# Kernel tuning notes

Hardware: AMD Instinct MI355X
Metric: run time of the kernel (lower is better)

The kernel has to match this reference:

```python
import jax, jax.numpy as jnp
import numpy as np

N = 100000      # nodes
E = 1600000     # edges (avg degree 16)
D_IN = 128
D_H = 128
D_OUT = 2


def setup_inputs() -> dict:
    key = jax.random.key(0)
    ks = jax.random.split(key, 13)
    s = 0.05
    x = jax.random.normal(ks[0], (N, D_IN), jnp.float32)
    edge_src = jax.random.randint(ks[1], (E,), 0, N, jnp.int32)
    edge_dst = jax.random.randint(ks[2], (E,), 0, N, jnp.int32)
    # SAGEConv params per layer: lin_l (aggregated path, with bias), lin_r (root path)
    w_l0 = jax.random.normal(ks[3], (D_H, D_IN), jnp.float32) * s
    b0 = jnp.zeros((D_H,), jnp.float32)
    w_r0 = jax.random.normal(ks[4], (D_H, D_IN), jnp.float32) * s
    w_l1 = jax.random.normal(ks[5], (D_H, D_H), jnp.float32) * s
    b1 = jnp.zeros((D_H,), jnp.float32)
    w_r1 = jax.random.normal(ks[6], (D_H, D_H), jnp.float32) * s
    w_l2 = jax.random.normal(ks[7], (D_OUT, D_H), jnp.float32) * s
    b2 = jnp.zeros((D_OUT,), jnp.float32)
    w_r2 = jax.random.normal(ks[8], (D_OUT, D_H), jnp.float32) * s
    return {"x": x, "w_l0": w_l0, "b0": b0, "w_r0": w_r0,
            "w_l1": w_l1, "b1": b1, "w_r1": w_r1,
            "w_l2": w_l2, "b2": b2, "w_r2": w_r2,
            "edge_src": edge_src, "edge_dst": edge_dst}


def _sage_conv(h, src, dst, inv_deg, w_l, b, w_r):
    # mean aggregation of neighbor features: gather -> segment_sum -> scale
    agg = jax.ops.segment_sum(h[src], dst, num_segments=N) * inv_deg  # [N, d_in]
    return agg @ w_l.T + b + h @ w_r.T


def reference(x, w_l0, b0, w_r0, w_l1, b1, w_r1, w_l2, b2, w_r2, edge_src, edge_dst):
    # in-degree for mean aggregation (0-degree nodes -> mean of 0)
    deg = jax.ops.segment_sum(jnp.ones((E,), jnp.float32), edge_dst, num_segments=N)
    inv_deg = (1.0 / jnp.maximum(deg, 1.0))[:, None]  # [N, 1]
    h = jax.nn.relu(_sage_conv(x, edge_src, edge_dst, inv_deg, w_l0, b0, w_r0))
    # dropout is identity at inference (training=False)
    h = jax.nn.relu(_sage_conv(h, edge_src, edge_dst, inv_deg, w_l1, b1, w_r1))
    out = _sage_conv(h, edge_src, edge_dst, inv_deg, w_l2, b2, w_r2)
    return jax.nn.log_softmax(out, axis=1)
```

## Files before the change

### kernel.cpp

```cpp
#include <hip/hip_runtime.h>
#include <stdint.h>
#include <stddef.h>

#define DH 128
#define CHUNK 4096
#define NBKMAX 128

typedef short v8s __attribute__((ext_vector_type(8)));
typedef float v4f __attribute__((ext_vector_type(4)));

static __device__ __forceinline__ float bf2f(uint16_t h) {
    union { uint32_t i; float f; } u; u.i = ((uint32_t)h) << 16; return u.f;
}
static __device__ __forceinline__ uint16_t f2bf(float f) {
    union { float f; uint32_t i; } u; u.f = f;
    uint32_t r = u.i + 0x7fffu + ((u.i >> 16) & 1u);
    return (uint16_t)(r >> 16);
}
static __device__ __forceinline__ float loadf(const void* p, size_t i, bool f32) {
    return f32 ? ((const float*)p)[i] : bf2f(((const uint16_t*)p)[i]);
}

__global__ void init_k(const uint32_t* w, int* flag) {
    int t = threadIdx.x;
    int hits = 0;
    for (int k = 0; k < 4; ++k) {
        uint32_t u = w[t * 4 + k];
        int e = (u >> 7) & 0xFF;
        hits += (e >= 100 && e <= 130) ? 1 : 0;
    }
    for (int off = 32; off; off >>= 1) hits += __shfl_down(hits, off);
    if (t == 0) *flag = (hits >= 128) ? 0 : 1;
}

__global__ void cvtall_k(const void* x, const void* wl0, const void* wr0,
                         const void* wl1, const void* wr1, const void* b0,
                         const void* b1, const int* dt, uint16_t* xb,
                         uint16_t* wcvt, int nx) {
    int i = blockIdx.x * 256 + threadIdx.x;
    bool f32 = (*dt != 0);
    if (i < nx) {
        if (f32) xb[i] = f2bf(((const float*)x)[i]);
        return;
    }
    int j = i - nx;
    const void* src; int off;
    if      (j < 16384) { src = wl0; off = j; }
    else if (j < 32768) { src = wr0; off = j - 16384; }
    else if (j < 49152) { src = wl1; off = j - 32768; }
    else if (j < 65536) { src = wr1; off = j - 49152; }
    else if (j < 65664) { src = b0;  off = j - 65536; }
    else if (j < 65792) { src = b1;  off = j - 65664; }
    else return;
    wcvt[j] = f32 ? f2bf(((const float*)src)[off]) : ((const uint16_t*)src)[off];
}

__global__ void histA_k(const int* __restrict__ dst, int* gh,
                        int E, int n, int GH, int nbk) {
    __shared__ int h[NBKMAX];
    int t = threadIdx.x;
    int base = blockIdx.x * CHUNK;
    for (int i = t; i < NBKMAX; i += 256) h[i] = 0;
    __syncthreads();
    for (int it = 0; it < CHUNK / 256; ++it) {
        int e = base + it * 256 + t;
        if (e < E) {
            int d = dst[e];
            if ((unsigned)d < (unsigned)n) atomicAdd(&h[d >> 10], 1);
        }
    }
    __syncthreads();
    for (int b = t; b < nbk; b += 256) gh[b * GH + blockIdx.x] = h[b];
}

__global__ void scan1_k(const int* cnt, int* bsum, int n) {
    __shared__ int wt[4];
    int t = threadIdx.x, lane = t & 63, wv = t >> 6;
    int i = blockIdx.x * 256 + t;
    int v = (i < n) ? cnt[i] : 0;
    for (int off = 32; off; off >>= 1) v += __shfl_down(v, off);
    if (lane == 0) wt[wv] = v;
    __syncthreads();
    if (t == 0) bsum[blockIdx.x] = wt[0] + wt[1] + wt[2] + wt[3];
}

__global__ void scan2_k(const int* bsum, int* boff, int* row_n, int nb) {
    __shared__ int wt[4];
    __shared__ int carry_s;
    int t = threadIdx.x, lane = t & 63, wv = t >> 6;
    if (t == 0) carry_s = 0;
    __syncthreads();
    for (int base = 0; base < nb; base += 256) {
        int i = base + t;
        int c = (i < nb) ? bsum[i] : 0;
        int v = c;
        for (int off = 1; off < 64; off <<= 1) {
            int u = __shfl_up(v, off);
            if (lane >= off) v += u;
        }
        if (lane == 63) wt[wv] = v;
        __syncthreads();
        int woff = 0;
        for (int w = 0; w < wv; ++w) woff += wt[w];
        int total = wt[0] + wt[1] + wt[2] + wt[3];
        int carry = carry_s;
        if (i < nb) boff[i] = carry + woff + (v - c);
        __syncthreads();
        if (t == 0) carry_s = carry + total;
        __syncthreads();
    }
    if (t == 0) *row_n = carry_s;
}

__global__ void scanG3_k(const int* in, const int* boff, int* out, int n) {
    __shared__ int wt[4];
    int t = threadIdx.x, lane = t & 63, wv = t >> 6;
    int i = blockIdx.x * 256 + t;
    int c = (i < n) ? in[i] : 0;
    int v = c;
    for (int off = 1; off < 64; off <<= 1) {
        int u = __shfl_up(v, off);
        if (lane >= off) v += u;
    }
    if (lane == 63) wt[wv] = v;
    __syncthreads();
    int woff = 0;
    for (int w = 0; w < wv; ++w) woff += wt[w];
    if (i < n) out[i] = boff[blockIdx.x] + woff + (v - c);
}

__global__ void scatB_k(const int* __restrict__ src, const int* __restrict__ dst,
                        const int* __restrict__ ghs, uint32_t* gbuf,
                        int E, int n, int GH, int nbk) {
    __shared__ int cur[NBKMAX];
    int t = threadIdx.x;
    int base = blockIdx.x * CHUNK;
    for (int b = t; b < nbk; b += 256) cur[b] = ghs[b * GH + blockIdx.x];
    __syncthreads();
    for (int it = 0; it < CHUNK / 256; ++it) {
        int e = base + it * 256 + t;
        if (e < E) {
            int d = dst[e];
            if ((unsigned)d < (unsigned)n) {
                int s = src[e];
                int slot = atomicAdd(&cur[d >> 10], 1);
                uint32_t rec = ((uint32_t)(d & 1023) << 17) | (uint32_t)s;
                __builtin_nontemporal_store(rec, &gbuf[slot]);
            }
        }
    }
}

__global__ void regroupC_k(const uint32_t* __restrict__ gbuf, const int* ghs,
                           const int* __restrict__ totalp, int GH,
                           int* row_start, float* inv_deg, int* csr_src,
                           int n, int nbk) {
    __shared__ int lcnt[1024];
    __shared__ int rs[1024];
    __shared__ int wsum[4];
    int b = blockIdx.x, t = threadIdx.x, lane = t & 63, wv = t >> 6;
    int node0 = b << 10;
    int nn = n - node0; if (nn > 1024) nn = 1024;
    int start = ghs[b * GH];
    int end = (b + 1 < nbk) ? ghs[(b + 1) * GH] : *totalp;
    for (int i = t; i < 1024; i += 256) lcnt[i] = 0;
    __syncthreads();
    for (int i = start + t; i < end; i += 256)
        atomicAdd(&lcnt[gbuf[i] >> 17], 1);
    __syncthreads();
    int c0 = lcnt[t * 4], c1 = lcnt[t * 4 + 1], c2 = lcnt[t * 4 + 2], c3 = lcnt[t * 4 + 3];
    int s = c0 + c1 + c2 + c3;
    int v = s;
    for (int off = 1; off < 64; off <<= 1) {
        int u = __shfl_up(v, off);
        if (lane >= off) v += u;
    }
    if (lane == 63) wsum[wv] = v;
    __syncthreads();
    int woff = 0;
    for (int w = 0; w < wv; ++w) woff += wsum[w];
    int ex = woff + (v - s);
    rs[t * 4]     = ex;
    rs[t * 4 + 1] = ex + c0;
    rs[t * 4 + 2] = ex + c0 + c1;
    rs[t * 4 + 3] = ex + c0 + c1 + c2;
    __syncthreads();
    for (int i = t; i < nn; i += 256) {
        row_start[node0 + i] = start + rs[i];
        inv_deg[node0 + i] = 1.0f / fmaxf((float)lcnt[i], 1.0f);
    }
    __syncthreads();
    for (int i = t; i < 1024; i += 256) lcnt[i] = 0;
    __syncthreads();
    for (int i = start + t; i < end; i += 256) {
        uint32_t rec = gbuf[i];
        int local = rec >> 17;
        int sv = rec & 0x1FFFF;
        int rank = atomicAdd(&lcnt[local], 1);
        csr_src[start + rs[local] + rank] = sv;
    }
}

__global__ void agg_k(const uint16_t* feat, const uint16_t* feat_alt, const int* xdt,
                      const int* csr_src, const int* row_start, const float* inv_deg,
                      uint16_t* A, int n) {
    int wave = threadIdx.x >> 6, lane = threadIdx.x & 63;
    int node = blockIdx.x * 4 + wave;
    if (node >= n) return;
    const uint16_t* f = feat;
    if (xdt != nullptr && *xdt == 0) f = feat_alt;
    int seg = lane & 7, sub = lane >> 3;
    int e0 = row_start[node], e1 = row_start[node + 1];
    const uint4* fp = (const uint4*)f;
    float acc[16];
#pragma unroll
    for (int i = 0; i < 16; ++i) acc[i] = 0.f;
    for (int e = e0 + sub; e < e1; e += 8) {
        int s = csr_src[e];
        if ((unsigned)s >= (unsigned)n) continue;
        const uint4* row = fp + (size_t)s * 16 + seg * 2;
        uint4 u0 = row[0];
        uint4 u1 = row[1];
        acc[0]  += bf2f((uint16_t)u0.x); acc[1]  += bf2f((uint16_t)(u0.x >> 16));
        acc[2]  += bf2f((uint16_t)u0.y); acc[3]  += bf2f((uint16_t)(u0.y >> 16));
        acc[4]  += bf2f((uint16_t)u0.z); acc[5]  += bf2f((uint16_t)(u0.z >> 16));
        acc[6]  += bf2f((uint16_t)u0.w); acc[7]  += bf2f((uint16_t)(u0.w >> 16));
        acc[8]  += bf2f((uint16_t)u1.x); acc[9]  += bf2f((uint16_t)(u1.x >> 16));
        acc[10] += bf2f((uint16_t)u1.y); acc[11] += bf2f((uint16_t)(u1.y >> 16));
        acc[12] += bf2f((uint16_t)u1.z); acc[13] += bf2f((uint16_t)(u1.z >> 16));
        acc[14] += bf2f((uint16_t)u1.w); acc[15] += bf2f((uint16_t)(u1.w >> 16));
    }
#pragma unroll
    for (int i = 0; i < 16; ++i) {
        acc[i] += __shfl_down(acc[i], 32);
        acc[i] += __shfl_down(acc[i], 16);
        acc[i] += __shfl_down(acc[i], 8);
    }
    if (sub == 0) {
        float sc = inv_deg[node];
        uint4 o0, o1;
        o0.x = (uint32_t)f2bf(acc[0]*sc)  | ((uint32_t)f2bf(acc[1]*sc)  << 16);
        o0.y = (uint32_t)f2bf(acc[2]*sc)  | ((uint32_t)f2bf(acc[3]*sc)  << 16);
        o0.z = (uint32_t)f2bf(acc[4]*sc)  | ((uint32_t)f2bf(acc[5]*sc)  << 16);
        o0.w = (uint32_t)f2bf(acc[6]*sc)  | ((uint32_t)f2bf(acc[7]*sc)  << 16);
        o1.x = (uint32_t)f2bf(acc[8]*sc)  | ((uint32_t)f2bf(acc[9]*sc)  << 16);
        o1.y = (uint32_t)f2bf(acc[10]*sc) | ((uint32_t)f2bf(acc[11]*sc) << 16);
        o1.z = (uint32_t)f2bf(acc[12]*sc) | ((uint32_t)f2bf(acc[13]*sc) << 16);
        o1.w = (uint32_t)f2bf(acc[14]*sc) | ((uint32_t)f2bf(acc[15]*sc) << 16);
        uint4* dst = (uint4*)A + (size_t)node * 16 + seg * 2;
        dst[0] = o0;
        dst[1] = o1;
    }
}

__global__ void dense2_k(const uint16_t* __restrict__ X,
                         const uint16_t* __restrict__ Xalt, const int* xdt,
                         const uint16_t* __restrict__ A,
                         const uint16_t* __restrict__ Wr,
                         const uint16_t* __restrict__ Wl,
                         const uint16_t* __restrict__ bias,
                         uint16_t* __restrict__ H, int n) {
    const int lane = threadIdx.x & 63;
    const int wv = threadIdx.x >> 6;
    const int m0 = blockIdx.x * 128 + wv * 32;
    if (m0 >= n) return;
    const uint16_t* Xs = X;
    if (xdt != nullptr && *xdt == 0) Xs = Xalt;
    const int row16 = lane & 15, quad = lane >> 4;
    int mr0 = m0 + row16;      int ml0 = (mr0 < n) ? mr0 : (n - 1);
    int mr1 = m0 + 16 + row16; int ml1 = (mr1 < n) ? mr1 : (n - 1);
    v8s ax0[4], aa0[4], ax1[4], aa1[4];
    const uint16_t* xr0 = Xs + (size_t)ml0 * DH + quad * 8;
    const uint16_t* ar0 = A  + (size_t)ml0 * DH + quad * 8;
    const uint16_t* xr1 = Xs + (size_t)ml1 * DH + quad * 8;
    const uint16_t* ar1 = A  + (size_t)ml1 * DH + quad * 8;
#pragma unroll
    for (int kt = 0; kt < 4; ++kt) {
        ax0[kt] = *(const v8s*)(xr0 + kt * 32);
        aa0[kt] = *(const v8s*)(ar0 + kt * 32);
        ax1[kt] = *(const v8s*)(xr1 + kt * 32);
        aa1[kt] = *(const v8s*)(ar1 + kt * 32);
    }
#pragma unroll
    for (int nt = 0; nt < 8; ++nt) {
        v4f acc0 = {0.f, 0.f, 0.f, 0.f};
        v4f acc1 = {0.f, 0.f, 0.f, 0.f};
        const uint16_t* wrr = Wr + (size_t)(nt * 16 + row16) * DH + quad * 8;
        const uint16_t* wlr = Wl + (size_t)(nt * 16 + row16) * DH + quad * 8;
#pragma unroll
        for (int kt = 0; kt < 4; ++kt) {
            v8s br = *(const v8s*)(wrr + kt * 32);
            acc0 = __builtin_amdgcn_mfma_f32_16x16x32_bf16(ax0[kt], br, acc0, 0, 0, 0);
            acc1 = __builtin_amdgcn_mfma_f32_16x16x32_bf16(ax1[kt], br, acc1, 0, 0, 0);
            v8s bl = *(const v8s*)(wlr + kt * 32);
            acc0 = __builtin_amdgcn_mfma_f32_16x16x32_bf16(aa0[kt], bl, acc0, 0, 0, 0);
            acc1 = __builtin_amdgcn_mfma_f32_16x16x32_bf16(aa1[kt], bl, acc1, 0, 0, 0);
        }
        int o = nt * 16 + row16;
        float bo = bf2f(bias[o]);
#pragma unroll
        for (int r = 0; r < 4; ++r) {
            int m = m0 + quad * 4 + r;
            if (m < n)
                H[(size_t)m * DH + o] = f2bf(fmaxf(acc0[r] + bo, 0.0f));
            int m2 = m0 + 16 + quad * 4 + r;
            if (m2 < n)
                H[(size_t)m2 * DH + o] = f2bf(fmaxf(acc1[r] + bo, 0.0f));
        }
    }
}

__global__ void transform2_k(const uint16_t* H, const void* Wl2,
                             const void* Wr2, const int* wdt,
                             float* T, float* Q, int n) {
    int wave = threadIdx.x >> 6, lane = threadIdx.x & 63;
    int node = blockIdx.x * 4 + wave;
    if (node >= n) return;
    bool f32 = (*wdt != 0);
    const uint16_t* h = H + (size_t)node * DH;
    float h0 = bf2f(h[lane]), h1 = bf2f(h[lane + 64]);
    float p0 = h0 * loadf(Wl2, lane, f32)       + h1 * loadf(Wl2, 64 + lane, f32);
    float p1 = h0 * loadf(Wl2, 128 + lane, f32) + h1 * loadf(Wl2, 192 + lane, f32);
    float q0 = h0 * loadf(Wr2, lane, f32)       + h1 * loadf(Wr2, 64 + lane, f32);
    float q1 = h0 * loadf(Wr2, 128 + lane, f32) + h1 * loadf(Wr2, 192 + lane, f32);
    for (int off = 32; off; off >>= 1) {
        p0 += __shfl_down(p0, off);
        p1 += __shfl_down(p1, off);
        q0 += __shfl_down(q0, off);
        q1 += __shfl_down(q1, off);
    }
    if (lane == 0) {
        T[(size_t)node * 2]     = p0;
        T[(size_t)node * 2 + 1] = p1;
        Q[(size_t)node * 2]     = q0;
        Q[(size_t)node * 2 + 1] = q1;
    }
}

__global__ void final_k(const float* T, const float* Q, const int* row_start,
                        const int* csr_src, const float* inv_deg,
                        const void* b2, const int* wdt, float* out, int n) {
    int i = blockIdx.x * 256 + threadIdx.x;
    if (i >= n) return;
    bool f32 = (*wdt != 0);
    int e0 = row_start[i], e1 = row_start[i + 1];
    float s0 = 0.f, s1 = 0.f;
    for (int e = e0; e < e1; ++e) {
        int j = csr_src[e];
        if ((unsigned)j >= (unsigned)n) continue;
        s0 += T[(size_t)j * 2];
        s1 += T[(size_t)j * 2 + 1];
    }
    float sc = inv_deg[i];
    float l0 = s0 * sc + loadf(b2, 0, f32) + Q[(size_t)i * 2];
    float l1 = s1 * sc + loadf(b2, 1, f32) + Q[(size_t)i * 2 + 1];
    float m = fmaxf(l0, l1);
    float lse = m + logf(expf(l0 - m) + expf(l1 - m));
    out[(size_t)i * 2]     = l0 - lse;
    out[(size_t)i * 2 + 1] = l1 - lse;
}

extern "C" void kernel_launch(void* const* d_in, const int* in_sizes, int n_in,
                              void* d_out, int out_size, void* d_ws, size_t ws_size,
                              hipStream_t stream) {
    int ix, iwl0, ib0, iwr0, iwl1, ib1, iwr1, iwl2, ib2, iwr2, iesrc, iedst;
    if (in_sizes[0] < 100000) {
        ib0 = 0; ib1 = 1; ib2 = 2; iedst = 3; iesrc = 4;
        iwl0 = 5; iwl1 = 6; iwl2 = 7; iwr0 = 8; iwr1 = 9; iwr2 = 10; ix = 11;
    } else {
        ix = 0; iwl0 = 1; ib0 = 2; iwr0 = 3; iwl1 = 4; ib1 = 5;
        iwr1 = 6; iwl2 = 7; ib2 = 8; iwr2 = 9; iesrc = 10; iedst = 11;
    }
    const void* x   = d_in[ix];
    const void* wl0 = d_in[iwl0];
    const void* b0  = d_in[ib0];
    const void* wr0 = d_in[iwr0];
    const void* wl1 = d_in[iwl1];
    const void* b1  = d_in[ib1];
    const void* wr1 = d_in[iwr1];
    const void* wl2 = d_in[iwl2];
    const void* b2  = d_in[ib2];
    const void* wr2 = d_in[iwr2];
    const int* esrc = (const int*)d_in[iesrc];
    const int* edst = (const int*)d_in[iedst];
    const int N = out_size / 2;
    const int E = in_sizes[iesrc];
    (void)n_in; (void)ws_size;

    char* ws = (char*)d_ws;
    size_t off = 0;
    auto carve = [&](size_t bytes) -> char* {
        char* p = ws + off;
        off = (off + bytes + 255) & ~(size_t)255;
        return p;
    };
    int gN = (N + 255) / 256;
    int GH = (E + CHUNK - 1) / CHUNK;
    int nbk = (N + 1023) >> 10;
    int n_scan = nbk * GH;
    int gS = (n_scan + 255) / 256;
    int* dtf        = (int*)   carve(256);
    int* gh         = (int*)   carve((size_t)n_scan * 4);
    int* ghs        = (int*)   carve((size_t)n_scan * 4);
    int* bsum       = (int*)   carve((size_t)gS * 4);
    int* boff       = (int*)   carve((size_t)gS * 4);
    uint32_t* gbuf  = (uint32_t*)carve((size_t)E * 4);
    int* row_start  = (int*)   carve((size_t)(N + 1) * 4);
    float* inv_deg  = (float*) carve((size_t)N * 4);
    int* csr_src    = (int*)   carve((size_t)E * 4);
    uint16_t* A16   = (uint16_t*)carve((size_t)N * DH * 2);
    uint16_t* H16   = (uint16_t*)carve((size_t)N * DH * 2);
    uint16_t* xb    = (uint16_t*)carve((size_t)N * DH * 2);
    uint16_t* wcvt  = (uint16_t*)carve(65792 * 2);
    float* T        = (float*) carve((size_t)N * 2 * 4);
    float* Q        = (float*) carve((size_t)N * 2 * 4);
    uint16_t* wl0b = wcvt;
    uint16_t* wr0b = wcvt + 16384;
    uint16_t* wl1b = wcvt + 32768;
    uint16_t* wr1b = wcvt + 49152;
    uint16_t* b0b  = wcvt + 65536;
    uint16_t* b1b  = wcvt + 65664;

    int ga = (N + 3) / 4;
    int gd = (N + 127) / 128;
    int nx = N * DH;
    int gc = (nx + 65792 + 255) / 256;

    init_k<<<1, 64, 0, stream>>>((const uint32_t*)wl0, dtf);
    cvtall_k<<<gc, 256, 0, stream>>>(x, wl0, wr0, wl1, wr1, b0, b1, dtf, xb, wcvt, nx);

    histA_k<<<GH, 256, 0, stream>>>(edst, gh, E, N, GH, nbk);
    scan1_k<<<gS, 256, 0, stream>>>(gh, bsum, n_scan);
    scan2_k<<<1, 256, 0, stream>>>(bsum, boff, &row_start[N], gS);
    scanG3_k<<<gS, 256, 0, stream>>>(gh, boff, ghs, n_scan);
    scatB_k<<<GH, 256, 0, stream>>>(esrc, edst, ghs, gbuf, E, N, GH, nbk);
    regroupC_k<<<nbk, 256, 0, stream>>>(gbuf, ghs, &row_start[N], GH,
                                        row_start, inv_deg, csr_src, N, nbk);

    agg_k<<<ga, 256, 0, stream>>>(xb, (const uint16_t*)x, dtf,
                                  csr_src, row_start, inv_deg, A16, N);
    dense2_k<<<gd, 256, 0, stream>>>(xb, (const uint16_t*)x, dtf,
                                     A16, wr0b, wl0b, b0b, H16, N);

    agg_k<<<ga, 256, 0, stream>>>(H16, nullptr, nullptr,
                                  csr_src, row_start, inv_deg, A16, N);
    dense2_k<<<gd, 256, 0, stream>>>(H16, nullptr, nullptr,
                                     A16, wr1b, wl1b, b1b, H16, N);

    transform2_k<<<ga, 256, 0, stream>>>(H16, wl2, wr2, dtf, T, Q, N);
    final_k<<<gN, 256, 0, stream>>>(T, Q, row_start, csr_src, inv_deg,
                                    b2, dtf, (float*)d_out, N);
}
```

Baseline: 472.5 us.

## Fuse dtype probe, last-layer projection and conversions; shrink bucket size to 512

Result: slower. 517.6 us (+9.5%).

```diff
diff --git a/kernel.cpp b/kernel.cpp
--- a/kernel.cpp
+++ b/kernel.cpp
@@ -4,7 +4,8 @@
 
 #define DH 128
 #define CHUNK 4096
-#define NBKMAX 128
+#define PBK_SHIFT 9
+#define NBKMAX 224
 
 typedef short v8s __attribute__((ext_vector_type(8)));
 typedef float v4f __attribute__((ext_vector_type(4)));
@@ -21,44 +22,20 @@
     return f32 ? ((const float*)p)[i] : bf2f(((const uint16_t*)p)[i]);
 }
 
-__global__ void init_k(const uint32_t* w, int* flag) {
-    int t = threadIdx.x;
-    int hits = 0;
-    for (int k = 0; k < 4; ++k) {
-        uint32_t u = w[t * 4 + k];
-        int e = (u >> 7) & 0xFF;
-        hits += (e >= 100 && e <= 130) ? 1 : 0;
-    }
-    for (int off = 32; off; off >>= 1) hits += __shfl_down(hits, off);
-    if (t == 0) *flag = (hits >= 128) ? 0 : 1;
-}
-
-__global__ void cvtall_k(const void* x, const void* wl0, const void* wr0,
-                         const void* wl1, const void* wr1, const void* b0,
-                         const void* b1, const int* dt, uint16_t* xb,
-                         uint16_t* wcvt, int nx) {
-    int i = blockIdx.x * 256 + threadIdx.x;
-    bool f32 = (*dt != 0);
-    if (i < nx) {
-        if (f32) xb[i] = f2bf(((const float*)x)[i]);
-        return;
-    }
-    int j = i - nx;
-    const void* src; int off;
-    if      (j < 16384) { src = wl0; off = j; }
-    else if (j < 32768) { src = wr0; off = j - 16384; }
-    else if (j < 49152) { src = wl1; off = j - 32768; }
-    else if (j < 65536) { src = wr1; off = j - 49152; }
-    else if (j < 65664) { src = b0;  off = j - 65536; }
-    else if (j < 65792) { src = b1;  off = j - 65664; }
-    else return;
-    wcvt[j] = f32 ? f2bf(((const float*)src)[off]) : ((const uint16_t*)src)[off];
-}
-
-__global__ void histA_k(const int* __restrict__ dst, int* gh,
-                        int E, int n, int GH, int nbk) {
+__global__ void histA_k(const int* __restrict__ dst, const uint32_t* w, int* flag,
+                        int* gh, int E, int n, int GH, int nbk) {
     __shared__ int h[NBKMAX];
     int t = threadIdx.x;
+    if (blockIdx.x == 0 && t < 64) {
+        int hits = 0;
+        for (int k = 0; k < 4; ++k) {
+            uint32_t u = w[t * 4 + k];
+            int e = (u >> 7) & 0xFF;
+            hits += (e >= 100 && e <= 130) ? 1 : 0;
+        }
+        for (int off = 32; off; off >>= 1) hits += __shfl_down(hits, off);
+        if (t == 0) *flag = (hits >= 128) ? 0 : 1;
+    }
     int base = blockIdx.x * CHUNK;
     for (int i = t; i < NBKMAX; i += 256) h[i] = 0;
     __syncthreads();
@@ -66,11 +43,33 @@
         int e = base + it * 256 + t;
         if (e < E) {
             int d = dst[e];
-            if ((unsigned)d < (unsigned)n) atomicAdd(&h[d >> 10], 1);
+            if ((unsigned)d < (unsigned)n) atomicAdd(&h[d >> PBK_SHIFT], 1);
         }
     }
     __syncthreads();
     for (int b = t; b < nbk; b += 256) gh[b * GH + blockIdx.x] = h[b];
+}
+
+__global__ void cvtall_k(const void* x, const void* wl0, const void* wr0,
+                         const void* wl1, const void* wr1, const void* b0,
+                         const void* b1, const int* dt, uint16_t* xb,
+                         uint16_t* wcvt, int nx, int nthr) {
+    int i = blockIdx.x * 256 + threadIdx.x;
+    bool f32 = (*dt != 0);
+    if (i < 65792) {
+        const void* src; int off;
+        if      (i < 16384) { src = wl0; off = i; }
+        else if (i < 32768) { src = wr0; off = i - 16384; }
+        else if (i < 49152) { src = wl1; off = i - 32768; }
+        else if (i < 65536) { src = wr1; off = i - 49152; }
+        else if (i < 65664) { src = b0;  off = i - 65536; }
+        else                { src = b1;  off = i - 65664; }
+        wcvt[i] = f32 ? f2bf(((const float*)src)[off]) : ((const uint16_t*)src)[off];
+    }
+    if (f32) {
+        for (int k = i; k < nx; k += nthr)
+            xb[k] = f2bf(((const float*)x)[k]);
+    }
 }
 
 __global__ void scan1_k(const int* cnt, int* bsum, int n) {
@@ -143,8 +142,8 @@
             int d = dst[e];
             if ((unsigned)d < (unsigned)n) {
                 int s = src[e];
-                int slot = atomicAdd(&cur[d >> 10], 1);
-                uint32_t rec = ((uint32_t)(d & 1023) << 17) | (uint32_t)s;
+                int slot = atomicAdd(&cur[d >> PBK_SHIFT], 1);
+                uint32_t rec = ((uint32_t)(d & 511) << 17) | (uint32_t)s;
                 __builtin_nontemporal_store(rec, &gbuf[slot]);
             }
         }
@@ -155,21 +154,21 @@
                            const int* __restrict__ totalp, int GH,
                            int* row_start, float* inv_deg, int* csr_src,
                            int n, int nbk) {
-    __shared__ int lcnt[1024];
-    __shared__ int rs[1024];
+    __shared__ int lcnt[512];
+    __shared__ int rs[512];
     __shared__ int wsum[4];
     int b = blockIdx.x, t = threadIdx.x, lane = t & 63, wv = t >> 6;
-    int node0 = b << 10;
-    int nn = n - node0; if (nn > 1024) nn = 1024;
+    int node0 = b << PBK_SHIFT;
+    int nn = n - node0; if (nn > 512) nn = 512;
     int start = ghs[b * GH];
     int end = (b + 1 < nbk) ? ghs[(b + 1) * GH] : *totalp;
-    for (int i = t; i < 1024; i += 256) lcnt[i] = 0;
+    for (int i = t; i < 512; i += 256) lcnt[i] = 0;
     __syncthreads();
     for (int i = start + t; i < end; i += 256)
         atomicAdd(&lcnt[gbuf[i] >> 17], 1);
     __syncthreads();
-    int c0 = lcnt[t * 4], c1 = lcnt[t * 4 + 1], c2 = lcnt[t * 4 + 2], c3 = lcnt[t * 4 + 3];
-    int s = c0 + c1 + c2 + c3;
+    int c0 = lcnt[2 * t], c1 = lcnt[2 * t + 1];
+    int s = c0 + c1;
     int v = s;
     for (int off = 1; off < 64; off <<= 1) {
         int u = __shfl_up(v, off);
@@ -180,17 +179,15 @@
     int woff = 0;
     for (int w = 0; w < wv; ++w) woff += wsum[w];
     int ex = woff + (v - s);
-    rs[t * 4]     = ex;
-    rs[t * 4 + 1] = ex + c0;
-    rs[t * 4 + 2] = ex + c0 + c1;
-    rs[t * 4 + 3] = ex + c0 + c1 + c2;
+    rs[2 * t]     = ex;
+    rs[2 * t + 1] = ex + c0;
     __syncthreads();
     for (int i = t; i < nn; i += 256) {
         row_start[node0 + i] = start + rs[i];
         inv_deg[node0 + i] = 1.0f / fmaxf((float)lcnt[i], 1.0f);
     }
     __syncthreads();
-    for (int i = t; i < 1024; i += 256) lcnt[i] = 0;
+    for (int i = t; i < 512; i += 256) lcnt[i] = 0;
     __syncthreads();
     for (int i = start + t; i < end; i += 256) {
         uint32_t rec = gbuf[i];
@@ -259,13 +256,17 @@
                          const uint16_t* __restrict__ Wr,
                          const uint16_t* __restrict__ Wl,
                          const uint16_t* __restrict__ bias,
-                         uint16_t* __restrict__ H, int n) {
+                         uint16_t* __restrict__ H,
+                         const void* wl2, const void* wr2, const int* wdt,
+                         float* T, float* Q, int n) {
     const int lane = threadIdx.x & 63;
     const int wv = threadIdx.x >> 6;
     const int m0 = blockIdx.x * 128 + wv * 32;
     if (m0 >= n) return;
     const uint16_t* Xs = X;
     if (xdt != nullptr && *xdt == 0) Xs = Xalt;
+    const bool tq = (T != nullptr);
+    const bool wf = tq && (*wdt != 0);
     const int row16 = lane & 15, quad = lane >> 4;
     int mr0 = m0 + row16;      int ml0 = (mr0 < n) ? mr0 : (n - 1);
     int mr1 = m0 + 16 + row16; int ml1 = (mr1 < n) ? mr1 : (n - 1);
@@ -281,6 +282,13 @@
         ax1[kt] = *(const v8s*)(xr1 + kt * 32);
         aa1[kt] = *(const v8s*)(ar1 + kt * 32);
     }
+    float tqa[4][8];
+    if (tq) {
+#pragma unroll
+        for (int a = 0; a < 4; ++a)
+#pragma unroll
+            for (int j = 0; j < 8; ++j) tqa[a][j] = 0.f;
+    }
 #pragma unroll
     for (int nt = 0; nt < 8; ++nt) {
         v4f acc0 = {0.f, 0.f, 0.f, 0.f};
@@ -298,42 +306,54 @@
         }
         int o = nt * 16 + row16;
         float bo = bf2f(bias[o]);
+        float wl2_0 = 0.f, wl2_1 = 0.f, wr2_0 = 0.f, wr2_1 = 0.f;
+        if (tq) {
+            wl2_0 = loadf(wl2, o, wf);  wl2_1 = loadf(wl2, 128 + o, wf);
+            wr2_0 = loadf(wr2, o, wf);  wr2_1 = loadf(wr2, 128 + o, wf);
+        }
 #pragma unroll
         for (int r = 0; r < 4; ++r) {
             int m = m0 + quad * 4 + r;
-            if (m < n)
-                H[(size_t)m * DH + o] = f2bf(fmaxf(acc0[r] + bo, 0.0f));
+            float h0 = fmaxf(acc0[r] + bo, 0.0f);
+            if (m < n) H[(size_t)m * DH + o] = f2bf(h0);
             int m2 = m0 + 16 + quad * 4 + r;
-            if (m2 < n)
-                H[(size_t)m2 * DH + o] = f2bf(fmaxf(acc1[r] + bo, 0.0f));
-        }
-    }
-}
-
-__global__ void transform2_k(const uint16_t* H, const void* Wl2,
-                             const void* Wr2, const int* wdt,
-                             float* T, float* Q, int n) {
-    int wave = threadIdx.x >> 6, lane = threadIdx.x & 63;
-    int node = blockIdx.x * 4 + wave;
-    if (node >= n) return;
-    bool f32 = (*wdt != 0);
-    const uint16_t* h = H + (size_t)node * DH;
-    float h0 = bf2f(h[lane]), h1 = bf2f(h[lane + 64]);
-    float p0 = h0 * loadf(Wl2, lane, f32)       + h1 * loadf(Wl2, 64 + lane, f32);
-    float p1 = h0 * loadf(Wl2, 128 + lane, f32) + h1 * loadf(Wl2, 192 + lane, f32);
-    float q0 = h0 * loadf(Wr2, lane, f32)       + h1 * loadf(Wr2, 64 + lane, f32);
-    float q1 = h0 * loadf(Wr2, 128 + lane, f32) + h1 * loadf(Wr2, 192 + lane, f32);
-    for (int off = 32; off; off >>= 1) {
-        p0 += __shfl_down(p0, off);
-        p1 += __shfl_down(p1, off);
-        q0 += __shfl_down(q0, off);
-        q1 += __shfl_down(q1, off);
-    }
-    if (lane == 0) {
-        T[(size_t)node * 2]     = p0;
-        T[(size_t)node * 2 + 1] = p1;
-        Q[(size_t)node * 2]     = q0;
-        Q[(size_t)node * 2 + 1] = q1;
+            float h1 = fmaxf(acc1[r] + bo, 0.0f);
+            if (m2 < n) H[(size_t)m2 * DH + o] = f2bf(h1);
+            if (tq) {
+                tqa[0][r] += h0 * wl2_0; tqa[1][r] += h0 * wl2_1;
+                tqa[2][r] += h0 * wr2_0; tqa[3][r] += h0 * wr2_1;
+                tqa[0][4 + r] += h1 * wl2_0; tqa[1][4 + r] += h1 * wl2_1;
+                tqa[2][4 + r] += h1 * wr2_0; tqa[3][4 + r] += h1 * wr2_1;
+            }
+        }
+    }
+    if (tq) {
+#pragma unroll
+        for (int mbit = 1; mbit < 16; mbit <<= 1)
+#pragma unroll
+            for (int a = 0; a < 4; ++a)
+#pragma unroll
+                for (int j = 0; j < 8; ++j)
+                    tqa[a][j] += __shfl_xor(tqa[a][j], mbit);
+        if (row16 == 0) {
+#pragma unroll
+            for (int r = 0; r < 4; ++r) {
+                int m = m0 + quad * 4 + r;
+                if (m < n) {
+                    T[(size_t)m * 2]     = tqa[0][r];
+                    T[(size_t)m * 2 + 1] = tqa[1][r];
+                    Q[(size_t)m * 2]     = tqa[2][r];
+                    Q[(size_t)m * 2 + 1] = tqa[3][r];
+                }
+                int m2 = m0 + 16 + quad * 4 + r;
+                if (m2 < n) {
+                    T[(size_t)m2 * 2]     = tqa[0][4 + r];
+                    T[(size_t)m2 * 2 + 1] = tqa[1][4 + r];
+                    Q[(size_t)m2 * 2]     = tqa[2][4 + r];
+                    Q[(size_t)m2 * 2 + 1] = tqa[3][4 + r];
+                }
+            }
+        }
     }
 }
 
@@ -345,11 +365,13 @@
     bool f32 = (*wdt != 0);
     int e0 = row_start[i], e1 = row_start[i + 1];
     float s0 = 0.f, s1 = 0.f;
+    const float2* T2 = (const float2*)T;
     for (int e = e0; e < e1; ++e) {
         int j = csr_src[e];
         if ((unsigned)j >= (unsigned)n) continue;
-        s0 += T[(size_t)j * 2];
-        s1 += T[(size_t)j * 2 + 1];
+        float2 tv = T2[j];
+        s0 += tv.x;
+        s1 += tv.y;
     }
     float sc = inv_deg[i];
     float l0 = s0 * sc + loadf(b2, 0, f32) + Q[(size_t)i * 2];
@@ -396,7 +418,7 @@
     };
     int gN = (N + 255) / 256;
     int GH = (E + CHUNK - 1) / CHUNK;
-    int nbk = (N + 1023) >> 10;
+    int nbk = (N + 511) >> PBK_SHIFT;
     int n_scan = nbk * GH;
     int gS = (n_scan + 255) / 256;
     int* dtf        = (int*)   carve(256);
@@ -424,12 +446,12 @@
     int ga = (N + 3) / 4;
     int gd = (N + 127) / 128;
     int nx = N * DH;
-    int gc = (nx + 65792 + 255) / 256;
-
-    init_k<<<1, 64, 0, stream>>>((const uint32_t*)wl0, dtf);
-    cvtall_k<<<gc, 256, 0, stream>>>(x, wl0, wr0, wl1, wr1, b0, b1, dtf, xb, wcvt, nx);
-
-    histA_k<<<GH, 256, 0, stream>>>(edst, gh, E, N, GH, nbk);
+    int gc = 257;
+
+    histA_k<<<GH, 256, 0, stream>>>(edst, (const uint32_t*)wl0, dtf, gh, E, N, GH, nbk);
+    cvtall_k<<<gc, 256, 0, stream>>>(x, wl0, wr0, wl1, wr1, b0, b1, dtf,
+                                     xb, wcvt, nx, gc * 256);
+
     scan1_k<<<gS, 256, 0, stream>>>(gh, bsum, n_scan);
     scan2_k<<<1, 256, 0, stream>>>(bsum, boff, &row_start[N], gS);
     scanG3_k<<<gS, 256, 0, stream>>>(gh, boff, ghs, n_scan);
@@ -440,14 +462,16 @@
     agg_k<<<ga, 256, 0, stream>>>(xb, (const uint16_t*)x, dtf,
                                   csr_src, row_start, inv_deg, A16, N);
     dense2_k<<<gd, 256, 0, stream>>>(xb, (const uint16_t*)x, dtf,
-                                     A16, wr0b, wl0b, b0b, H16, N);
+                                     A16, wr0b, wl0b, b0b, H16,
+                                     nullptr, nullptr, nullptr,
+                                     nullptr, nullptr, N);
 
     agg_k<<<ga, 256, 0, stream>>>(H16, nullptr, nullptr,
                                   csr_src, row_start, inv_deg, A16, N);
     dense2_k<<<gd, 256, 0, stream>>>(H16, nullptr, nullptr,
-                                     A16, wr1b, wl1b, b1b, H16, N);
-
-    transform2_k<<<ga, 256, 0, stream>>>(H16, wl2, wr2, dtf, T, Q, N);
+                                     A16, wr1b, wl1b, b1b, H16,
+                                     wl2, wr2, dtf, T, Q, N);
+
     final_k<<<gN, 256, 0, stream>>>(T, Q, row_start, csr_src, inv_deg,
                                     b2, dtf, (float*)d_out, N);
 }
```
